# Kernel optimization log

Hardware: AMD Instinct MI355X
Metric: run time of the kernel (lower is better)

The kernel has to match this reference:

```python
import jax, jax.numpy as jnp
import numpy as np

EMBED_DIM = 768
NUM_HEADS = 12
HEAD_DIM = EMBED_DIM // NUM_HEADS
SCALE = HEAD_DIM ** -0.5


def setup_inputs() -> dict:
    key = jax.random.key(0)
    k1, k2, k3, k4, k5 = jax.random.split(key, 5)
    B, T = 8, 1024
    hidden_states = jax.random.normal(k1, (B, T, EMBED_DIM), dtype=jnp.float32)
    init = 0.02
    qkv_w = jax.random.normal(k2, (EMBED_DIM, 3 * EMBED_DIM), dtype=jnp.float32) * init
    qkv_b = jnp.zeros((3 * EMBED_DIM,), dtype=jnp.float32)
    proj_w = jax.random.normal(k3, (EMBED_DIM, EMBED_DIM), dtype=jnp.float32) * init
    proj_b = jnp.zeros((EMBED_DIM,), dtype=jnp.float32)
    return {
        "hidden_states": hidden_states,
        "qkv_w": qkv_w,
        "qkv_b": qkv_b,
        "proj_w": proj_w,
        "proj_b": proj_b,
    }


def reference(hidden_states, qkv_w, qkv_b, proj_w, proj_b):
    B, T, C = hidden_states.shape
    # fused QKV projection
    mixed = hidden_states @ qkv_w + qkv_b            # [B, T, 3C]
    mixed = mixed.reshape(B, T, 3, NUM_HEADS, HEAD_DIM)
    mixed = jnp.transpose(mixed, (2, 0, 3, 1, 4))    # [3, B, H, T, D]
    q, k, v = mixed[0], mixed[1], mixed[2]
    # scaled dot-product attention (dropout is identity in eval)
    scores = jnp.einsum("bhqd,bhkd->bhqk", q, k) * SCALE
    probs = jax.nn.softmax(scores, axis=-1)
    ctx = jnp.einsum("bhqk,bhkd->bhqd", probs, v)    # [B, H, T, D]
    ctx = jnp.transpose(ctx, (0, 2, 1, 3)).reshape(B, T, C)
    out = ctx @ proj_w + proj_b
    return out
```

## Files before the change

kernel.cpp:

```cpp
#include <hip/hip_runtime.h>

#define EMBED 768
#define NHEAD 12
#define HDIM 64
#define BATCH 8
#define SEQ 1024
#define ROWS (BATCH*SEQ)
#define QKVN (3*EMBED)
#define ATTN_SCALE 0.125f

typedef short s16x8 __attribute__((ext_vector_type(8)));
typedef float f32x4 __attribute__((ext_vector_type(4)));

__device__ __forceinline__ float bf2f(unsigned short u) {
    union { unsigned int i; float f; } v; v.i = ((unsigned int)u) << 16; return v.f;
}
__device__ __forceinline__ unsigned short f2bf(float f) {
    unsigned int i = __builtin_bit_cast(unsigned int, f);
    i += 0x7FFFu + ((i >> 16) & 1u);
    return (unsigned short)(i >> 16);
}

__device__ __forceinline__ void async16(short* lds, const unsigned short* g) {
    __builtin_amdgcn_global_load_lds(
        (const __attribute__((address_space(1))) unsigned int*)g,
        (__attribute__((address_space(3))) unsigned int*)lds,
        16, 0, 0);
}

__global__ __launch_bounds__(256) void prep_k(
    const float* __restrict__ qkv_w, unsigned short* __restrict__ WqkvT,
    const float* __restrict__ proj_w, unsigned short* __restrict__ WprojT,
    const float* __restrict__ hidden, unsigned short* __restrict__ hiddenBf)
{
    __shared__ float tile[64][65];
    int blk = blockIdx.x;
    int t = threadIdx.x;
    if (blk < 576) {
        const float* in; unsigned short* outp; int K, N, tx, ty;
        if (blk < 432) { in = qkv_w; outp = WqkvT; K = EMBED; N = QKVN; tx = blk % 36; ty = blk / 36; }
        else { int b2 = blk - 432; in = proj_w; outp = WprojT; K = EMBED; N = EMBED; tx = b2 % 12; ty = b2 / 12; }
        int n0 = tx * 64, k0 = ty * 64;
        int c = t & 63, r0 = t >> 6;
        #pragma unroll
        for (int i = 0; i < 16; i++) {
            int r = r0 * 16 + i;
            tile[r][c] = in[(long long)(k0 + r) * N + n0 + c];
        }
        __syncthreads();
        #pragma unroll
        for (int i = 0; i < 16; i++) {
            int nr = r0 * 16 + i;
            outp[(long long)(n0 + nr) * K + k0 + c] = f2bf(tile[c][nr]);
        }
    } else {
        int tid = (blk - 576) * 256 + t;
        int base = tid * 8;
        float4 f0 = *(const float4*)&hidden[base];
        float4 f1 = *(const float4*)&hidden[base + 4];
        s16x8 a;
        a[0] = (short)f2bf(f0.x); a[1] = (short)f2bf(f0.y);
        a[2] = (short)f2bf(f0.z); a[3] = (short)f2bf(f0.w);
        a[4] = (short)f2bf(f1.x); a[5] = (short)f2bf(f1.y);
        a[6] = (short)f2bf(f1.z); a[7] = (short)f2bf(f1.w);
        *(s16x8*)&hiddenBf[base] = a;
    }
}

template <int OUT_F32>
__global__ __launch_bounds__(256) void gemm128(
    const unsigned short* __restrict__ A,
    const unsigned short* __restrict__ Bt,
    const float* __restrict__ bias,
    void* __restrict__ Cv,
    int M, int N, int K)
{
    __shared__ short As[128 * 32];
    __shared__ short Bs[128 * 32];
    int t = threadIdx.x, lane = t & 63, w = t >> 6;
    int quad = lane >> 4, low = lane & 15;
    int m0 = blockIdx.x * 128, n0 = blockIdx.y * 128;
    int wm = (w & 1) * 64, wn = (w >> 1) * 64;

    int ci0 = w * 128 + lane;
    int r0 = ci0 >> 2, c0 = (ci0 & 3) ^ ((r0 >> 1) & 3);
    int ci1 = ci0 + 64;
    int r1 = ci1 >> 2, c1 = (ci1 & 3) ^ ((r1 >> 1) & 3);
    const unsigned short* pa0 = A + (long long)(m0 + r0) * K + c0 * 8;
    const unsigned short* pa1 = A + (long long)(m0 + r1) * K + c1 * 8;
    const unsigned short* pb0 = Bt + (long long)(n0 + r0) * K + c0 * 8;
    const unsigned short* pb1 = Bt + (long long)(n0 + r1) * K + c1 * 8;
    short* la0 = As + (w * 128) * 8;
    short* la1 = As + (w * 128 + 64) * 8;
    short* lb0 = Bs + (w * 128) * 8;
    short* lb1 = Bs + (w * 128 + 64) * 8;

    f32x4 acc[4][4] = {};
    for (int k0 = 0; k0 < K; k0 += 32) {
        __syncthreads();
        async16(la0, pa0 + k0);
        async16(la1, pa1 + k0);
        async16(lb0, pb0 + k0);
        async16(lb1, pb1 + k0);
        __syncthreads();
        s16x8 af[4], bfr[4];
        #pragma unroll
        for (int i = 0; i < 4; i++) {
            int ra = wm + i * 16 + low;
            af[i] = *(const s16x8*)&As[ra * 32 + ((quad ^ ((ra >> 1) & 3)) * 8)];
            int rb = wn + i * 16 + low;
            bfr[i] = *(const s16x8*)&Bs[rb * 32 + ((quad ^ ((rb >> 1) & 3)) * 8)];
        }
        #pragma unroll
        for (int i = 0; i < 4; i++)
            #pragma unroll
            for (int j = 0; j < 4; j++)
                acc[i][j] = __builtin_amdgcn_mfma_f32_16x16x32_bf16(af[i], bfr[j], acc[i][j], 0, 0, 0);
    }
    #pragma unroll
    for (int i = 0; i < 4; i++)
        #pragma unroll
        for (int j = 0; j < 4; j++)
            #pragma unroll
            for (int r = 0; r < 4; r++) {
                int m = m0 + wm + i * 16 + quad * 4 + r;
                int n = n0 + wn + j * 16 + low;
                float v = acc[i][j][r] + bias[n];
                if (OUT_F32) ((float*)Cv)[(long long)m * N + n] = v;
                else ((unsigned short*)Cv)[(long long)m * N + n] = f2bf(v);
            }
}

__global__ __launch_bounds__(256) void attn_k(
    const unsigned short* __restrict__ mixed,
    unsigned short* __restrict__ ctx)
{
    __shared__ short Ks[64 * 72];
    __shared__ short Vt[64 * 72];
    __shared__ short Pl[4 * 32 * 72];
    int blk = blockIdx.x;
    int qc = blk & 7;
    int bh = blk >> 3;
    int b = bh / NHEAD, h = bh - b * NHEAD;
    int t = threadIdx.x;
    int lane = t & 63, w = t >> 6;
    int quad = lane >> 4, low = lane & 15;
    long long rowbase = (long long)b * SEQ;
    int q0 = qc * 128 + w * 32;
    int hoff = h * HDIM;

    s16x8 qf[2][2];
    #pragma unroll
    for (int qh = 0; qh < 2; qh++) {
        long long r = (rowbase + q0 + qh * 16 + low) * QKVN + hoff;
        qf[qh][0] = *(const s16x8*)&mixed[r + quad * 8];
        qf[qh][1] = *(const s16x8*)&mixed[r + 32 + quad * 8];
    }

    f32x4 o[2][4] = {};
    float lsum[2][4] = {};

    int skv = t >> 2;
    int sd = (t & 3) * 16;

    for (int kv0 = 0; kv0 < SEQ; kv0 += 64) {
        __syncthreads();
        long long krow = (rowbase + kv0 + skv) * QKVN + EMBED + hoff + sd;
        *(s16x8*)&Ks[skv * 72 + sd]     = *(const s16x8*)&mixed[krow];
        *(s16x8*)&Ks[skv * 72 + sd + 8] = *(const s16x8*)&mixed[krow + 8];
        long long vrow = (rowbase + kv0 + skv) * QKVN + 2 * EMBED + hoff + sd;
        s16x8 v0 = *(const s16x8*)&mixed[vrow];
        s16x8 v1 = *(const s16x8*)&mixed[vrow + 8];
        #pragma unroll
        for (int i = 0; i < 8; i++) {
            int d = sd + i;
            Vt[d * 72 + (skv ^ (((d >> 3) & 7) << 3))] = v0[i];
        }
        #pragma unroll
        for (int i = 0; i < 8; i++) {
            int d = sd + 8 + i;
            Vt[d * 72 + (skv ^ (((d >> 3) & 7) << 3))] = v1[i];
        }
        __syncthreads();

        f32x4 s[2][4] = {};
        #pragma unroll
        for (int n = 0; n < 4; n++) {
            s16x8 b0 = *(const s16x8*)&Ks[(n * 16 + low) * 72 + quad * 8];
            s16x8 b1 = *(const s16x8*)&Ks[(n * 16 + low) * 72 + 32 + quad * 8];
            s[0][n] = __builtin_amdgcn_mfma_f32_16x16x32_bf16(qf[0][0], b0, s[0][n], 0, 0, 0);
            s[0][n] = __builtin_amdgcn_mfma_f32_16x16x32_bf16(qf[0][1], b1, s[0][n], 0, 0, 0);
            s[1][n] = __builtin_amdgcn_mfma_f32_16x16x32_bf16(qf[1][0], b0, s[1][n], 0, 0, 0);
            s[1][n] = __builtin_amdgcn_mfma_f32_16x16x32_bf16(qf[1][1], b1, s[1][n], 0, 0, 0);
        }

        short* pw = &Pl[w * 32 * 72];
        #pragma unroll
        for (int qh = 0; qh < 2; qh++)
            #pragma unroll
            for (int n = 0; n < 4; n++)
                #pragma unroll
                for (int r = 0; r < 4; r++) {
                    float e = __expf(s[qh][n][r] * ATTN_SCALE);
                    lsum[qh][r] += e;
                    pw[(qh * 16 + quad * 4 + r) * 72 + n * 16 + low] = (short)f2bf(e);
                }

        s16x8 pf[2][2];
        #pragma unroll
        for (int qh = 0; qh < 2; qh++) {
            pf[qh][0] = *(const s16x8*)&pw[(qh * 16 + low) * 72 + quad * 8];
            pf[qh][1] = *(const s16x8*)&pw[(qh * 16 + low) * 72 + 32 + quad * 8];
        }

        #pragma unroll
        for (int nt = 0; nt < 4; nt++) {
            int d = nt * 16 + low;
            int key = (d >> 3) & 7;
            s16x8 vf0 = *(const s16x8*)&Vt[d * 72 + ((quad ^ key) << 3)];
            s16x8 vf1 = *(const s16x8*)&Vt[d * 72 + (((4 + quad) ^ key) << 3)];
            o[0][nt] = __builtin_amdgcn_mfma_f32_16x16x32_bf16(pf[0][0], vf0, o[0][nt], 0, 0, 0);
            o[0][nt] = __builtin_amdgcn_mfma_f32_16x16x32_bf16(pf[0][1], vf1, o[0][nt], 0, 0, 0);
            o[1][nt] = __builtin_amdgcn_mfma_f32_16x16x32_bf16(pf[1][0], vf0, o[1][nt], 0, 0, 0);
            o[1][nt] = __builtin_amdgcn_mfma_f32_16x16x32_bf16(pf[1][1], vf1, o[1][nt], 0, 0, 0);
        }
    }

    #pragma unroll
    for (int off = 1; off < 16; off <<= 1)
        #pragma unroll
        for (int qh = 0; qh < 2; qh++)
            #pragma unroll
            for (int r = 0; r < 4; r++)
                lsum[qh][r] += __shfl_xor(lsum[qh][r], off, 64);

    #pragma unroll
    for (int qh = 0; qh < 2; qh++)
        #pragma unroll
        for (int nt = 0; nt < 4; nt++)
            #pragma unroll
            for (int r = 0; r < 4; r++) {
                int q = q0 + qh * 16 + quad * 4 + r;
                ctx[(rowbase + q) * EMBED + hoff + nt * 16 + low] =
                    f2bf(o[qh][nt][r] / lsum[qh][r]);
            }
}

extern "C" void kernel_launch(void* const* d_in, const int* in_sizes, int n_in,
                              void* d_out, int out_size, void* d_ws, size_t ws_size,
                              hipStream_t stream) {
    const float* hidden = (const float*)d_in[0];
    const float* qkv_w  = (const float*)d_in[1];
    const float* qkv_b  = (const float*)d_in[2];
    const float* proj_w = (const float*)d_in[3];
    const float* proj_b = (const float*)d_in[4];
    float* out = (float*)d_out;

    char* ws = (char*)d_ws;
    unsigned short* hiddenBf = (unsigned short*)ws;
    unsigned short* ctx      = (unsigned short*)ws;
    unsigned short* WqkvT    = (unsigned short*)(ws + 12582912);
    unsigned short* WprojT   = (unsigned short*)(ws + 16121856);
    unsigned short* mixed    = (unsigned short*)(ws + 17301504);

    prep_k<<<dim3(3648), 256, 0, stream>>>(qkv_w, WqkvT, proj_w, WprojT, hidden, hiddenBf);
    gemm128<0><<<dim3(ROWS / 128, QKVN / 128), 256, 0, stream>>>(
        hiddenBf, WqkvT, qkv_b, mixed, ROWS, QKVN, EMBED);
    attn_k<<<dim3(96 * 8), 256, 0, stream>>>(mixed, ctx);
    gemm128<1><<<dim3(ROWS / 128, EMBED / 128), 256, 0, stream>>>(
        ctx, WprojT, proj_b, out, ROWS, EMBED, EMBED);
}
```

Measured before the change: 207.0 us.

## Restructure attention inner loop: transposed scores, register P, async K loads

The attention kernel now computes S^T, so the exp'd probabilities come out of the MFMA accumulator already in the operand layout needed by a 16x16x16 bf16 MFMA. This removes the per-wave LDS round-trip for P. K tiles are loaded with async global-to-LDS copies into an XOR-swizzled buffer, and V is transposed through a 4x4 register shuffle with vector LDS stores. The change also adds s_setprio around the MFMA blocks, packs bf16 conversions into single instructions, swaps the block index order so heads vary fastest, and simplifies the row-sum reduction. The P-operand path now runs twice as many narrower MFMAs, and the kernel still has no max subtraction in the softmax.

Result: faster. 198.5 us (-4.1%).

```diff
diff --git a/kernel.cpp b/kernel.cpp
--- a/kernel.cpp
+++ b/kernel.cpp
@@ -10,6 +10,7 @@
 #define ATTN_SCALE 0.125f
 
 typedef short s16x8 __attribute__((ext_vector_type(8)));
+typedef short s16x4 __attribute__((ext_vector_type(4)));
 typedef float f32x4 __attribute__((ext_vector_type(4)));
 
 __device__ __forceinline__ float bf2f(unsigned short u) {
@@ -26,6 +27,15 @@
         (const __attribute__((address_space(1))) unsigned int*)g,
         (__attribute__((address_space(3))) unsigned int*)lds,
         16, 0, 0);
+}
+
+__device__ __forceinline__ f32x4 mfma16(s16x4 a, s16x4 b, f32x4 c) {
+#if __has_builtin(__builtin_amdgcn_mfma_f32_16x16x16bf16_1k)
+    return __builtin_amdgcn_mfma_f32_16x16x16bf16_1k(a, b, c, 0, 0, 0);
+#else
+    asm volatile("v_mfma_f32_16x16x16_bf16 %0, %1, %2, %0" : "+v"(c) : "v"(a), "v"(b));
+    return c;
+#endif
 }
 
 __global__ __launch_bounds__(256) void prep_k(
@@ -135,12 +145,11 @@
     const unsigned short* __restrict__ mixed,
     unsigned short* __restrict__ ctx)
 {
-    __shared__ short Ks[64 * 72];
-    __shared__ short Vt[64 * 72];
-    __shared__ short Pl[4 * 32 * 72];
+    __shared__ short Ks[64 * 64];
+    __shared__ short Vt[64 * 68];
     int blk = blockIdx.x;
-    int qc = blk & 7;
-    int bh = blk >> 3;
+    int bh = blk % 96;
+    int qc = blk / 96;
     int b = bh / NHEAD, h = bh - b * NHEAD;
     int t = threadIdx.x;
     int lane = t & 63, w = t >> 6;
@@ -157,93 +166,100 @@
         qf[qh][1] = *(const s16x8*)&mixed[r + 32 + quad * 8];
     }
 
+    int s0 = w * 128 + lane;
+    int kr0 = s0 >> 3, kc0 = s0 & 7;
+    int kg = kc0 ^ (kr0 & 7);
+    const unsigned short* pk0 = mixed + (rowbase + kr0) * QKVN + EMBED + hoff + kg * 8;
+    const unsigned short* pk1 = mixed + (rowbase + kr0 + 8) * QKVN + EMBED + hoff + kg * 8;
+    short* lk0 = Ks + (w * 128) * 8;
+    short* lk1 = Ks + (w * 128 + 64) * 8;
+
+    int dblk = t & 15, rq = t >> 4;
+    const unsigned short* pv = mixed + (rowbase + rq * 4) * QKVN + 2 * EMBED + hoff + dblk * 4;
+
     f32x4 o[2][4] = {};
-    float lsum[2][4] = {};
-
-    int skv = t >> 2;
-    int sd = (t & 3) * 16;
+    float lsum[2] = {0.f, 0.f};
 
     for (int kv0 = 0; kv0 < SEQ; kv0 += 64) {
-        __syncthreads();
-        long long krow = (rowbase + kv0 + skv) * QKVN + EMBED + hoff + sd;
-        *(s16x8*)&Ks[skv * 72 + sd]     = *(const s16x8*)&mixed[krow];
-        *(s16x8*)&Ks[skv * 72 + sd + 8] = *(const s16x8*)&mixed[krow + 8];
-        long long vrow = (rowbase + kv0 + skv) * QKVN + 2 * EMBED + hoff + sd;
-        s16x8 v0 = *(const s16x8*)&mixed[vrow];
-        s16x8 v1 = *(const s16x8*)&mixed[vrow + 8];
-        #pragma unroll
-        for (int i = 0; i < 8; i++) {
-            int d = sd + i;
-            Vt[d * 72 + (skv ^ (((d >> 3) & 7) << 3))] = v0[i];
-        }
-        #pragma unroll
-        for (int i = 0; i < 8; i++) {
-            int d = sd + 8 + i;
-            Vt[d * 72 + (skv ^ (((d >> 3) & 7) << 3))] = v1[i];
-        }
-        __syncthreads();
-
-        f32x4 s[2][4] = {};
+        long long koff = (long long)kv0 * QKVN;
+        __syncthreads();
+        async16(lk0, pk0 + koff);
+        async16(lk1, pk1 + koff);
+        s16x4 v0 = *(const s16x4*)&pv[koff];
+        s16x4 v1 = *(const s16x4*)&pv[koff + QKVN];
+        s16x4 v2 = *(const s16x4*)&pv[koff + 2 * QKVN];
+        s16x4 v3 = *(const s16x4*)&pv[koff + 3 * QKVN];
+        #pragma unroll
+        for (int k = 0; k < 4; k++) {
+            s16x4 wv;
+            wv[0] = v0[k]; wv[1] = v1[k]; wv[2] = v2[k]; wv[3] = v3[k];
+            *(s16x4*)&Vt[(dblk * 4 + k) * 68 + rq * 4] = wv;
+        }
+        __syncthreads();
+
+        f32x4 sT[2][4] = {};
+        __builtin_amdgcn_s_setprio(1);
         #pragma unroll
         for (int n = 0; n < 4; n++) {
-            s16x8 b0 = *(const s16x8*)&Ks[(n * 16 + low) * 72 + quad * 8];
-            s16x8 b1 = *(const s16x8*)&Ks[(n * 16 + low) * 72 + 32 + quad * 8];
-            s[0][n] = __builtin_amdgcn_mfma_f32_16x16x32_bf16(qf[0][0], b0, s[0][n], 0, 0, 0);
-            s[0][n] = __builtin_amdgcn_mfma_f32_16x16x32_bf16(qf[0][1], b1, s[0][n], 0, 0, 0);
-            s[1][n] = __builtin_amdgcn_mfma_f32_16x16x32_bf16(qf[1][0], b0, s[1][n], 0, 0, 0);
-            s[1][n] = __builtin_amdgcn_mfma_f32_16x16x32_bf16(qf[1][1], b1, s[1][n], 0, 0, 0);
-        }
-
-        short* pw = &Pl[w * 32 * 72];
+            int rr = n * 16 + low;
+            int key = low & 7;
+            s16x8 kf0 = *(const s16x8*)&Ks[rr * 64 + ((quad ^ key) * 8)];
+            s16x8 kf1 = *(const s16x8*)&Ks[rr * 64 + (((quad + 4) ^ key) * 8)];
+            sT[0][n] = __builtin_amdgcn_mfma_f32_16x16x32_bf16(kf0, qf[0][0], sT[0][n], 0, 0, 0);
+            sT[0][n] = __builtin_amdgcn_mfma_f32_16x16x32_bf16(kf1, qf[0][1], sT[0][n], 0, 0, 0);
+            sT[1][n] = __builtin_amdgcn_mfma_f32_16x16x32_bf16(kf0, qf[1][0], sT[1][n], 0, 0, 0);
+            sT[1][n] = __builtin_amdgcn_mfma_f32_16x16x32_bf16(kf1, qf[1][1], sT[1][n], 0, 0, 0);
+        }
+        __builtin_amdgcn_s_setprio(0);
+
+        s16x4 pf[2][4];
         #pragma unroll
         for (int qh = 0; qh < 2; qh++)
             #pragma unroll
-            for (int n = 0; n < 4; n++)
-                #pragma unroll
-                for (int r = 0; r < 4; r++) {
-                    float e = __expf(s[qh][n][r] * ATTN_SCALE);
-                    lsum[qh][r] += e;
-                    pw[(qh * 16 + quad * 4 + r) * 72 + n * 16 + low] = (short)f2bf(e);
-                }
-
-        s16x8 pf[2][2];
-        #pragma unroll
-        for (int qh = 0; qh < 2; qh++) {
-            pf[qh][0] = *(const s16x8*)&pw[(qh * 16 + low) * 72 + quad * 8];
-            pf[qh][1] = *(const s16x8*)&pw[(qh * 16 + low) * 72 + 32 + quad * 8];
-        }
-
+            for (int n = 0; n < 4; n++) {
+                float e0 = __expf(sT[qh][n][0] * ATTN_SCALE);
+                float e1 = __expf(sT[qh][n][1] * ATTN_SCALE);
+                float e2 = __expf(sT[qh][n][2] * ATTN_SCALE);
+                float e3 = __expf(sT[qh][n][3] * ATTN_SCALE);
+                lsum[qh] += (e0 + e1) + (e2 + e3);
+                unsigned int w0, w1;
+                asm("v_cvt_pk_bf16_f32 %0, %1, %2" : "=v"(w0) : "v"(e0), "v"(e1));
+                asm("v_cvt_pk_bf16_f32 %0, %1, %2" : "=v"(w1) : "v"(e2), "v"(e3));
+                union { unsigned int u[2]; s16x4 v; } pu;
+                pu.u[0] = w0; pu.u[1] = w1;
+                pf[qh][n] = pu.v;
+            }
+
+        __builtin_amdgcn_s_setprio(1);
         #pragma unroll
         for (int nt = 0; nt < 4; nt++) {
-            int d = nt * 16 + low;
-            int key = (d >> 3) & 7;
-            s16x8 vf0 = *(const s16x8*)&Vt[d * 72 + ((quad ^ key) << 3)];
-            s16x8 vf1 = *(const s16x8*)&Vt[d * 72 + (((4 + quad) ^ key) << 3)];
-            o[0][nt] = __builtin_amdgcn_mfma_f32_16x16x32_bf16(pf[0][0], vf0, o[0][nt], 0, 0, 0);
-            o[0][nt] = __builtin_amdgcn_mfma_f32_16x16x32_bf16(pf[0][1], vf1, o[0][nt], 0, 0, 0);
-            o[1][nt] = __builtin_amdgcn_mfma_f32_16x16x32_bf16(pf[1][0], vf0, o[1][nt], 0, 0, 0);
-            o[1][nt] = __builtin_amdgcn_mfma_f32_16x16x32_bf16(pf[1][1], vf1, o[1][nt], 0, 0, 0);
-        }
-    }
-
-    #pragma unroll
-    for (int off = 1; off < 16; off <<= 1)
-        #pragma unroll
-        for (int qh = 0; qh < 2; qh++)
-            #pragma unroll
-            for (int r = 0; r < 4; r++)
-                lsum[qh][r] += __shfl_xor(lsum[qh][r], off, 64);
-
+            int drow = nt * 16 + low;
+            #pragma unroll
+            for (int n = 0; n < 4; n++) {
+                s16x4 vf = *(const s16x4*)&Vt[drow * 68 + n * 16 + quad * 4];
+                o[0][nt] = mfma16(pf[0][n], vf, o[0][nt]);
+                o[1][nt] = mfma16(pf[1][n], vf, o[1][nt]);
+            }
+        }
+        __builtin_amdgcn_s_setprio(0);
+    }
+
+    #pragma unroll
+    for (int qh = 0; qh < 2; qh++) {
+        lsum[qh] += __shfl_xor(lsum[qh], 16, 64);
+        lsum[qh] += __shfl_xor(lsum[qh], 32, 64);
+    }
     #pragma unroll
     for (int qh = 0; qh < 2; qh++)
         #pragma unroll
-        for (int nt = 0; nt < 4; nt++)
-            #pragma unroll
-            for (int r = 0; r < 4; r++) {
-                int q = q0 + qh * 16 + quad * 4 + r;
+        for (int r = 0; r < 4; r++) {
+            float inv = 1.0f / __shfl(lsum[qh], quad * 4 + r, 64);
+            int q = q0 + qh * 16 + quad * 4 + r;
+            #pragma unroll
+            for (int nt = 0; nt < 4; nt++)
                 ctx[(rowbase + q) * EMBED + hoff + nt * 16 + low] =
-                    f2bf(o[qh][nt][r] / lsum[qh][r]);
-            }
+                    f2bf(o[qh][nt][r] * inv);
+        }
 }
 
 extern "C" void kernel_launch(void* const* d_in, const int* in_sizes, int n_in,
```
